# Kernel tuning notes

Measured on AMD Instinct MI355X. Metric: run time of the kernel, lower is better.

## Reference

```python
import jax, jax.numpy as jnp
import numpy as np

# dims (match init_kwargs)
B, S, HID = 2, 2048, 2048
NH = 16
DN = 128   # qk_nope_head_dim
DR = 64    # qk_rope_head_dim
DV = 128   # v_head_dim
QLR = 1536 # q_lora_rank
KVLR = 512 # kv_lora_rank
QHD = DN + DR  # 192
ROPE_BASE = 10000.0
EPS = 1e-6


def rms_norm(x, w):
    # ZeroCenteredRMSNorm: weight is zero-centered, scale = (1 + w)
    var = jnp.mean(x * x, axis=-1, keepdims=True)
    return x * jax.lax.rsqrt(var + EPS) * (1.0 + w)


def rotate_half(x):
    d = x.shape[-1] // 2
    return jnp.concatenate([-x[..., d:], x[..., :d]], axis=-1)


def deinterleave(x):
    # rearrange '(d_pairs two) -> (two d_pairs)'
    return jnp.concatenate([x[..., 0::2], x[..., 1::2]], axis=-1)


def setup_inputs() -> dict:
    key = jax.random.key(0)
    ks = jax.random.split(key, 8)
    s = 0.02
    return {
        "hidden_states": jax.random.normal(ks[0], (B, S, HID), jnp.float32),
        "position_ids": jnp.arange(S, dtype=jnp.int32),
        "Wq_down": jax.random.normal(ks[1], (HID, QLR), jnp.float32) * s,
        "q_norm_w": jnp.zeros((QLR,), jnp.float32),
        "Wq_up": jax.random.normal(ks[2], (QLR, NH * QHD), jnp.float32) * s,
        "Wkv_down": jax.random.normal(ks[3], (HID, KVLR + DR), jnp.float32) * s,
        "kv_norm_w": jnp.zeros((KVLR,), jnp.float32),
        "Wkv_up": jax.random.normal(ks[4], (KVLR, NH * (DN + DV)), jnp.float32) * s,
        "W_gate": jax.random.normal(ks[5], (HID, NH * DV), jnp.float32) * s,
        "W_out": jax.random.normal(ks[6], (NH * DV, HID), jnp.float32) * s,
    }


def reference(hidden_states, position_ids, Wq_down, q_norm_w, Wq_up,
              Wkv_down, kv_norm_w, Wkv_up, W_gate, W_out):
    bsz, q_len, _ = hidden_states.shape
    pos = jnp.broadcast_to(position_ids[None, :], (bsz, q_len))  # [b,s]

    # Q path: down-proj -> RMSNorm -> up-proj -> [b,h,s,QHD]
    q = rms_norm(hidden_states @ Wq_down, q_norm_w) @ Wq_up
    q = q.reshape(bsz, q_len, NH, QHD).transpose(0, 2, 1, 3)
    q_nope, q_rope = q[..., :DN], q[..., DN:]

    # KV path: joint down-proj -> split latent / rope key
    ckv = hidden_states @ Wkv_down                     # [b,s,KVLR+DR]
    c_kv, k_rope = ckv[..., :KVLR], ckv[..., KVLR:]
    k_rope = k_rope[:, None, :, :]                     # [b,1,s,DR]
    kv = rms_norm(c_kv, kv_norm_w) @ Wkv_up            # [b,s,NH*(DN+DV)]
    kv = kv.reshape(bsz, q_len, NH, DN + DV).transpose(0, 2, 1, 3)
    k_nope, v = kv[..., :DN], kv[..., DN:]

    # partial RoPE on rope dims (with the '(pairs two)->(two pairs)' permute)
    inv_freq = 1.0 / (ROPE_BASE ** (jnp.arange(0, DR, 2, dtype=jnp.float32) / DR))
    freqs = pos[..., None].astype(jnp.float32) * inv_freq  # [b,s,DR/2]
    emb = jnp.concatenate([freqs, freqs], axis=-1)          # [b,s,DR]
    cos = jnp.cos(emb)[:, None, :, :]                       # [b,1,s,DR]
    sin = jnp.sin(emb)[:, None, :, :]
    q_r = deinterleave(q_rope)
    k_r = deinterleave(k_rope)
    q_r = q_r * cos + rotate_half(q_r) * sin
    k_r = k_r * cos + rotate_half(k_r) * sin

    query = jnp.concatenate([q_nope, q_r], axis=-1)                       # [b,h,s,QHD]
    key = jnp.concatenate([k_nope, jnp.broadcast_to(k_r, k_nope.shape[:-1] + (DR,))], axis=-1)

    scores = jnp.einsum('bhqd,bhkd->bhqk', query, key) / np.sqrt(QHD)
    attn = jax.nn.softmax(scores, axis=-1)
    out = jnp.einsum('bhqk,bhkd->bhqd', attn, v)                          # [b,h,s,DV]
    out = out.transpose(0, 2, 1, 3)                                       # [b,s,h,DV]

    gate = jax.nn.sigmoid(hidden_states @ W_gate).reshape(bsz, q_len, NH, DV)
    out = (out * gate).reshape(bsz, q_len, NH * DV)
    return out @ W_out
```

## Files before the change

kernel.cpp:

```cpp
#include <hip/hip_runtime.h>
#include <math.h>

#define BT 2
#define SL 2048
#define HIDN 2048
#define NHEADS 16
#define DNOPE 128
#define DROPE 64
#define DVAL 128
#define QHEAD 192
#define QLRANK 1536
#define KVLRANK 512
#define TTOK (BT * SL)
#define FN 4224
#define FC_CKV 1536
#define FC_ROPE 2048
#define FC_GATE 2176

typedef unsigned short u16;
typedef u16 u16x4 __attribute__((ext_vector_type(4)));
typedef u16 u16x8 __attribute__((ext_vector_type(8)));
typedef short bf16x8 __attribute__((ext_vector_type(8)));
typedef float f32x4 __attribute__((ext_vector_type(4)));

__device__ __forceinline__ u16 f2b(float f) {
    union { float f; unsigned u; } v; v.f = f;
    unsigned r = v.u + 0x7FFFu + ((v.u >> 16) & 1u);
    return (u16)(r >> 16);
}
__device__ __forceinline__ float b2f(u16 h) {
    union { unsigned u; float f; } v; v.u = ((unsigned)h) << 16;
    return v.f;
}

__device__ __forceinline__ void gl2lds16(const u16* g, u16* l) {
    __builtin_amdgcn_global_load_lds((const __attribute__((address_space(1))) unsigned int*)g,
                                     (__attribute__((address_space(3))) unsigned int*)l, 16, 0, 0);
}

__global__ __launch_bounds__(256) void cast_k(const float* __restrict__ in, u16* __restrict__ out,
                                              int n4) {
    int i = blockIdx.x * 256 + threadIdx.x;
    const int stride = gridDim.x * 256;
    for (; i < n4; i += stride) {
        const float4 v = ((const float4*)in)[i];
        u16x4 u;
        u.x = f2b(v.x); u.y = f2b(v.y); u.z = f2b(v.z); u.w = f2b(v.w);
        ((u16x4*)out)[i] = u;
    }
}

__device__ __forceinline__ void tcast_tile(const float* __restrict__ in, u16* __restrict__ out,
                                           int R, int C, int tx, int ty, int t) {
    __shared__ u16 tile[64][72];
    const int c0 = tx * 64, r0 = ty * 64;
    const int tr = t >> 4, tc4 = (t & 15) * 4;
#pragma unroll
    for (int i = 0; i < 4; ++i) {
        const int r = tr + i * 16;
        const float4 v = *(const float4*)&in[(size_t)(r0 + r) * C + c0 + tc4];
        u16x4 u;
        u.x = f2b(v.x); u.y = f2b(v.y); u.z = f2b(v.z); u.w = f2b(v.w);
        *(u16x4*)&tile[r][tc4] = u;
    }
    __syncthreads();
#pragma unroll
    for (int i = 0; i < 4; ++i) {
        const int rr = tr + i * 16;
        u16x4 u;
        u.x = tile[tc4 + 0][rr];
        u.y = tile[tc4 + 1][rr];
        u.z = tile[tc4 + 2][rr];
        u.w = tile[tc4 + 3][rr];
        *(u16x4*)&out[(size_t)(c0 + rr) * R + r0 + tc4] = u;
    }
}

__global__ __launch_bounds__(256) void tcast_all_k(
    const float* __restrict__ Wq_down, const float* __restrict__ Wq_up,
    const float* __restrict__ Wkv_down, const float* __restrict__ Wkv_up,
    const float* __restrict__ W_gate, const float* __restrict__ W_out, u16* __restrict__ wqd_t,
    u16* __restrict__ wqu_t, u16* __restrict__ wkvd_t, u16* __restrict__ wkvu_t,
    u16* __restrict__ wg_t, u16* __restrict__ wo_t) {
    const int tid = blockIdx.x;
    const int t = threadIdx.x;
    if (tid < 768) {
        tcast_tile(Wq_down, wqd_t, 2048, 1536, tid % 24, tid / 24, t);
    } else if (tid < 1920) {
        const int i = tid - 768;
        tcast_tile(Wq_up, wqu_t, 1536, 3072, i % 48, i / 48, t);
    } else if (tid < 2208) {
        const int i = tid - 1920;
        tcast_tile(Wkv_down, wkvd_t, 2048, 576, i % 9, i / 9, t);
    } else if (tid < 2720) {
        const int i = tid - 2208;
        tcast_tile(Wkv_up, wkvu_t, 512, 4096, i % 64, i / 64, t);
    } else if (tid < 3744) {
        const int i = tid - 2720;
        tcast_tile(W_gate, wg_t, 2048, 2048, i % 32, i / 32, t);
    } else {
        const int i = tid - 3744;
        tcast_tile(W_out, wo_t, 2048, 2048, i % 32, i / 32, t);
    }
}

__global__ __launch_bounds__(256) void vtrans_k(const u16* __restrict__ kvbuf,
                                                u16* __restrict__ vT) {
    __shared__ u16 tile[64][72];
    const int bh = blockIdx.z;
    const int b = bh >> 4, h = bh & 15;
    const int s0 = blockIdx.x * 64, d0 = blockIdx.y * 64;
    const int t = threadIdx.x;
    const int tr = t >> 4, tc4 = (t & 15) * 4;
#pragma unroll
    for (int i = 0; i < 4; ++i) {
        const int s = tr + i * 16;
        *(u16x4*)&tile[s][tc4] =
            *(const u16x4*)&kvbuf[(size_t)(b * SL + s0 + s) * 4096 + h * 256 + 128 + d0 + tc4];
    }
    __syncthreads();
#pragma unroll
    for (int i = 0; i < 4; ++i) {
        const int dd = tr + i * 16;
        u16x4 u;
        u.x = tile[tc4 + 0][dd];
        u.y = tile[tc4 + 1][dd];
        u.z = tile[tc4 + 2][dd];
        u.w = tile[tc4 + 3][dd];
        *(u16x4*)&vT[(size_t)(bh * 128 + d0 + dd) * SL + s0 + tc4] = u;
    }
}

template <int EPI, int OUTF>
__global__ __launch_bounds__(256) void gemm_bf16_k(const u16* __restrict__ A,
                                                   const u16* __restrict__ Bt,
                                                   void* __restrict__ Cv, int M, int N, int K) {
    __shared__ u16 As[128 * 64];
    __shared__ u16 Bs[128 * 64];
    const int t = threadIdx.x;
    const int nx = gridDim.x;
    const int bid = blockIdx.x + nx * blockIdx.y;
    const int cpx = (nx * gridDim.y) >> 3;
    const int swz = (bid & 7) * cpx + (bid >> 3);
    const int bn = (swz % nx) * 128, bm = (swz / nx) * 128;
    const int w = t >> 6, lane = t & 63;
    const int wr = (w >> 1) * 64, wc = (w & 1) * 64;
    const int lr = lane & 15, lg = lane >> 4;

    const int srow = w * 32 + (lane >> 3);
    const int scol = ((lane & 7) ^ ((lane >> 3) & 7)) * 8;
    const u16* Ag = A + (size_t)(bm + srow) * K + scol;
    const u16* Bg = Bt + (size_t)(bn + srow) * K + scol;
    u16* Asl = As + w * 2048;
    u16* Bsl = Bs + w * 2048;

    f32x4 acc[4][4];
#pragma unroll
    for (int i = 0; i < 4; ++i)
#pragma unroll
        for (int j = 0; j < 4; ++j) acc[i][j] = 0.f;

    for (int k0 = 0; k0 < K; k0 += 64) {
        __syncthreads();
#pragma unroll
        for (int j = 0; j < 4; ++j) gl2lds16(Ag + (size_t)(j * 8) * K + k0, Asl + j * 512);
#pragma unroll
        for (int j = 0; j < 4; ++j) gl2lds16(Bg + (size_t)(j * 8) * K + k0, Bsl + j * 512);
        __syncthreads();
#pragma unroll
        for (int kk = 0; kk < 2; ++kk) {
            bf16x8 af[4], bfr[4];
#pragma unroll
            for (int mi = 0; mi < 4; ++mi) {
                const int row = wr + mi * 16 + lr;
                const int idx = (row * 64 + kk * 32 + lg * 8) ^ ((row & 7) << 3);
                af[mi] = *(const bf16x8*)&As[idx];
            }
#pragma unroll
            for (int ni = 0; ni < 4; ++ni) {
                const int row = wc + ni * 16 + lr;
                const int idx = (row * 64 + kk * 32 + lg * 8) ^ ((row & 7) << 3);
                bfr[ni] = *(const bf16x8*)&Bs[idx];
            }
#pragma unroll
            for (int mi = 0; mi < 4; ++mi)
#pragma unroll
                for (int ni = 0; ni < 4; ++ni)
                    acc[mi][ni] = __builtin_amdgcn_mfma_f32_16x16x32_bf16(af[mi], bfr[ni],
                                                                          acc[mi][ni], 0, 0, 0);
        }
    }
#pragma unroll
    for (int mi = 0; mi < 4; ++mi)
#pragma unroll
        for (int ni = 0; ni < 4; ++ni)
#pragma unroll
            for (int r = 0; r < 4; ++r) {
                const int row = bm + wr + mi * 16 + lg * 4 + r;
                const int col = bn + wc + ni * 16 + lr;
                float v = acc[mi][ni][r];
                if (EPI == 1) v = 1.f / (1.f + __expf(-v));
                if (EPI == 2 && col >= FC_GATE) v = 1.f / (1.f + __expf(-v));
                if (col < N) {
                    if (OUTF)
                        ((float*)Cv)[(size_t)row * N + col] = v;
                    else
                        ((u16*)Cv)[(size_t)row * N + col] = f2b(v);
                }
            }
}

__global__ __launch_bounds__(256) void rms2_k(const u16* __restrict__ fout,
                                              const float* __restrict__ qw,
                                              const float* __restrict__ kw, u16* __restrict__ qn,
                                              u16* __restrict__ kvn) {
    const int rid = blockIdx.x;
    const bool isq = rid < TTOK;
    const int row = isq ? rid : rid - TTOK;
    const int n = isq ? QLRANK : KVLRANK;
    const u16* x = fout + (size_t)row * FN + (isq ? 0 : FC_CKV);
    const float* w = isq ? qw : kw;
    u16* y = isq ? (qn + (size_t)row * QLRANK) : (kvn + (size_t)row * KVLRANK);
    const int t = threadIdx.x;
    float ss = 0.f;
    for (int d = t * 4; d < n; d += 1024) {
        const u16x4 u = *(const u16x4*)&x[d];
        const float a = b2f(u.x), b = b2f(u.y), c = b2f(u.z), e = b2f(u.w);
        ss += a * a + b * b + c * c + e * e;
    }
    ss += __shfl_down(ss, 32);
    ss += __shfl_down(ss, 16);
    ss += __shfl_down(ss, 8);
    ss += __shfl_down(ss, 4);
    ss += __shfl_down(ss, 2);
    ss += __shfl_down(ss, 1);
    __shared__ float red[5];
    if ((t & 63) == 0) red[t >> 6] = ss;
    __syncthreads();
    if (t == 0) red[4] = rsqrtf((red[0] + red[1] + red[2] + red[3]) / (float)n + 1e-6f);
    __syncthreads();
    const float sc = red[4];
    for (int d = t * 4; d < n; d += 1024) {
        const u16x4 u = *(const u16x4*)&x[d];
        const float4 wv = *(const float4*)&w[d];
        u16x4 o;
        o.x = f2b(b2f(u.x) * sc * (1.f + wv.x));
        o.y = f2b(b2f(u.y) * sc * (1.f + wv.y));
        o.z = f2b(b2f(u.z) * sc * (1.f + wv.z));
        o.w = f2b(b2f(u.w) * sc * (1.f + wv.w));
        *(u16x4*)&y[d] = o;
    }
}

__global__ __launch_bounds__(64) void rope_k(u16* __restrict__ q, const u16* __restrict__ fout,
                                             u16* __restrict__ kr, const int* __restrict__ pos_ids) {
    const int tok = blockIdx.x * 2 + (threadIdx.x >> 5);
    const int j = threadIdx.x & 31;
    const int s = tok & (SL - 1);
    const float pos = (float)pos_ids[s];
    const float inv = 1.f / powf(10000.f, (float)(2 * j) / 64.f);
    const float f = pos * inv;
    const float c = cosf(f), sn = sinf(f);
    const u16* kc = fout + (size_t)tok * FN + FC_ROPE;
    const unsigned kp = *(const unsigned*)&kc[2 * j];
    const float ke = b2f((u16)(kp & 0xffff)), ko = b2f((u16)(kp >> 16));
    kr[tok * 64 + j] = f2b(ke * c - ko * sn);
    kr[tok * 64 + 32 + j] = f2b(ko * c + ke * sn);
#pragma unroll
    for (int h = 0; h < NHEADS; ++h) {
        u16* qb = q + (size_t)tok * (NHEADS * QHEAD) + h * QHEAD + DNOPE;
        const unsigned qp = *(const unsigned*)&qb[2 * j];
        const float qe = b2f((u16)(qp & 0xffff)), qo = b2f((u16)(qp >> 16));
        qb[j] = f2b(qe * c - qo * sn);
        qb[32 + j] = f2b(qo * c + qe * sn);
    }
}

#define PSTR 76
__global__ __launch_bounds__(256, 2) void mla_attn_k(const u16* __restrict__ qbuf,
                                                     const u16* __restrict__ kvbuf,
                                                     const u16* __restrict__ kr,
                                                     const u16* __restrict__ vT,
                                                     const u16* __restrict__ gateb,
                                                     u16* __restrict__ outg) {
    __shared__ u16 Ks[64 * 200];
    __shared__ u16 Vt[128 * 72];
    __shared__ u16 Ps[4 * 32 * PSTR];
    const int bh = blockIdx.x;
    const int b = bh >> 4, h = bh & 15;
    const int q0 = blockIdx.y * 128;
    const int t = threadIdx.x, w = t >> 6, lane = t & 63;
    const int lr = lane & 15, lg = lane >> 4;
    const float scale = 0.07216878364870322f;

    int kRow[6], kC8[6];
#pragma unroll
    for (int c = 0; c < 6; ++c) {
        const int i = t + c * 256;
        kRow[c] = i / 24;
        kC8[c] = (i % 24) * 8;
    }
    int vRow[4], vC8[4];
#pragma unroll
    for (int c = 0; c < 4; ++c) {
        const int i = t + c * 256;
        vRow[c] = i >> 3;
        vC8[c] = (i & 7) * 8;
    }

    bf16x8 aq[2][6];
#pragma unroll
    for (int mi = 0; mi < 2; ++mi) {
        const int qrow = b * SL + q0 + w * 32 + mi * 16 + lr;
#pragma unroll
        for (int ks = 0; ks < 6; ++ks)
            aq[mi][ks] =
                *(const bf16x8*)&qbuf[(size_t)qrow * (NHEADS * QHEAD) + h * QHEAD + ks * 32 + lg * 8];
    }

    f32x4 O[2][8];
#pragma unroll
    for (int mi = 0; mi < 2; ++mi)
#pragma unroll
        for (int df = 0; df < 8; ++df) O[mi][df] = 0.f;
    float m[2][4], l[2][4];
#pragma unroll
    for (int mi = 0; mi < 2; ++mi)
#pragma unroll
        for (int r = 0; r < 4; ++r) {
            m[mi][r] = -INFINITY;
            l[mi][r] = 0.f;
        }

    u16x8 kreg[6], vreg[4];
#define ATTN_ISSUE_K(K0)                                                                     \
    {                                                                                        \
        _Pragma("unroll") for (int c = 0; c < 6; ++c) {                                      \
            const int tok = b * SL + (K0) + kRow[c];                                         \
            kreg[c] = (kC8[c] < 128)                                                         \
                          ? *(const u16x8*)&kvbuf[(size_t)tok * 4096 + h * 256 + kC8[c]]     \
                          : *(const u16x8*)&kr[(size_t)tok * 64 + (kC8[c] - 128)];           \
        }                                                                                    \
    }
#define ATTN_ISSUE_V(K0)                                                                     \
    {                                                                                        \
        _Pragma("unroll") for (int c = 0; c < 4; ++c)                                        \
            vreg[c] = *(const u16x8*)&vT[(size_t)(bh * 128 + vRow[c]) * SL + (K0) + vC8[c]]; \
    }

    ATTN_ISSUE_K(0);
    ATTN_ISSUE_V(0);

    for (int it = 0; it < SL / 64; ++it) {
        __syncthreads();
#pragma unroll
        for (int c = 0; c < 6; ++c) *(u16x8*)&Ks[kRow[c] * 200 + kC8[c]] = kreg[c];
#pragma unroll
        for (int c = 0; c < 4; ++c) *(u16x8*)&Vt[vRow[c] * 72 + vC8[c]] = vreg[c];
        __syncthreads();
        const bool more = (it + 1) < SL / 64;
        const int kn = (it + 1) * 64;
        if (more) ATTN_ISSUE_K(kn);

        f32x4 s[2][4];
#pragma unroll
        for (int mi = 0; mi < 2; ++mi)
#pragma unroll
            for (int nf = 0; nf < 4; ++nf) s[mi][nf] = 0.f;
#pragma unroll
        for (int ks = 0; ks < 6; ++ks) {
#pragma unroll
            for (int nf = 0; nf < 4; ++nf) {
                const bf16x8 bk = *(const bf16x8*)&Ks[(nf * 16 + lr) * 200 + ks * 32 + lg * 8];
                s[0][nf] = __builtin_amdgcn_mfma_f32_16x16x32_bf16(aq[0][ks], bk, s[0][nf], 0, 0, 0);
                s[1][nf] = __builtin_amdgcn_mfma_f32_16x16x32_bf16(aq[1][ks], bk, s[1][nf], 0, 0, 0);
            }
        }

        float lmv[2][4];
        float growth = -INFINITY;
#pragma unroll
        for (int mi = 0; mi < 2; ++mi)
#pragma unroll
            for (int r = 0; r < 4; ++r) {
                float lm = fmaxf(fmaxf(s[mi][0][r], s[mi][1][r]), fmaxf(s[mi][2][r], s[mi][3][r])) * scale;
                lm = fmaxf(lm, __shfl_xor(lm, 1));
                lm = fmaxf(lm, __shfl_xor(lm, 2));
                lm = fmaxf(lm, __shfl_xor(lm, 4));
                lm = fmaxf(lm, __shfl_xor(lm, 8));
                lmv[mi][r] = lm;
                growth = fmaxf(growth, lm - m[mi][r]);
            }
        const bool skip = __all(growth <= 8.f);

#pragma unroll
        for (int mi = 0; mi < 2; ++mi) {
            const int pb = w * 32 * PSTR + mi * 16 * PSTR;
#pragma unroll
            for (int r = 0; r < 4; ++r) {
                const float mn = skip ? m[mi][r] : fmaxf(m[mi][r], lmv[mi][r]);
                float p0 = __expf(s[mi][0][r] * scale - mn);
                float p1 = __expf(s[mi][1][r] * scale - mn);
                float p2 = __expf(s[mi][2][r] * scale - mn);
                float p3 = __expf(s[mi][3][r] * scale - mn);
                float ps = (p0 + p1) + (p2 + p3);
                ps += __shfl_xor(ps, 1);
                ps += __shfl_xor(ps, 2);
                ps += __shfl_xor(ps, 4);
                ps += __shfl_xor(ps, 8);
                if (skip) {
                    l[mi][r] += ps;
                } else {
                    const float al = __expf(m[mi][r] - mn);
                    l[mi][r] = l[mi][r] * al + ps;
                    m[mi][r] = mn;
#pragma unroll
                    for (int df = 0; df < 8; ++df) O[mi][df][r] *= al;
                }
                const int prow = pb + (lg * 4 + r) * PSTR + lr;
                Ps[prow] = f2b(p0);
                Ps[prow + 16] = f2b(p1);
                Ps[prow + 32] = f2b(p2);
                Ps[prow + 48] = f2b(p3);
            }
        }

        if (more) ATTN_ISSUE_V(kn);

        bf16x8 pa[2][2];
#pragma unroll
        for (int mi = 0; mi < 2; ++mi)
#pragma unroll
            for (int ks2 = 0; ks2 < 2; ++ks2)
                pa[mi][ks2] =
                    *(const bf16x8*)&Ps[w * 32 * PSTR + (mi * 16 + lr) * PSTR + ks2 * 32 + lg * 8];
#pragma unroll
        for (int df = 0; df < 8; ++df)
#pragma unroll
            for (int ks2 = 0; ks2 < 2; ++ks2) {
                const bf16x8 bv = *(const bf16x8*)&Vt[(df * 16 + lr) * 72 + ks2 * 32 + lg * 8];
                O[0][df] = __builtin_amdgcn_mfma_f32_16x16x32_bf16(pa[0][ks2], bv, O[0][df], 0, 0, 0);
                O[1][df] = __builtin_amdgcn_mfma_f32_16x16x32_bf16(pa[1][ks2], bv, O[1][df], 0, 0, 0);
            }
    }
#pragma unroll
    for (int mi = 0; mi < 2; ++mi) {
        float invl[4];
#pragma unroll
        for (int r = 0; r < 4; ++r) invl[r] = 1.f / l[mi][r];
#pragma unroll
        for (int df = 0; df < 8; ++df)
#pragma unroll
            for (int r = 0; r < 4; ++r) {
                const int qq = b * SL + q0 + w * 32 + mi * 16 + lg * 4 + r;
                const int col = h * DVAL + df * 16 + lr;
                const float o = O[mi][df][r] * invl[r];
                const float g = b2f(gateb[(size_t)qq * FN + col]);
                outg[(size_t)qq * (NHEADS * DVAL) + col] = f2b(o * g);
            }
    }
}

extern "C" void kernel_launch(void* const* d_in, const int* in_sizes, int n_in, void* d_out,
                              int out_size, void* d_ws, size_t ws_size, hipStream_t stream) {
    const float* hs = (const float*)d_in[0];
    const int* pos = (const int*)d_in[1];
    const float* Wq_down = (const float*)d_in[2];
    const float* q_norm_w = (const float*)d_in[3];
    const float* Wq_up = (const float*)d_in[4];
    const float* Wkv_down = (const float*)d_in[5];
    const float* kv_norm_w = (const float*)d_in[6];
    const float* Wkv_up = (const float*)d_in[7];
    const float* W_gate = (const float*)d_in[8];
    const float* W_out = (const float*)d_in[9];
    float* out = (float*)d_out;

    u16* p = (u16*)d_ws;
    u16* hs16 = p;      p += (size_t)TTOK * HIDN;
    u16* wdown_t = p;   p += (size_t)FN * HIDN;
    u16* wqd_t = wdown_t;
    u16* wkvd_t = wdown_t + (size_t)QLRANK * HIDN;
    u16* wg_t = wdown_t + (size_t)FC_GATE * HIDN;
    u16* wqu_t = p;     p += (size_t)(NHEADS * QHEAD) * QLRANK;
    u16* wkvu_t = p;    p += (size_t)(NHEADS * 256) * KVLRANK;
    u16* wo_t = p;      p += (size_t)HIDN * (NHEADS * DVAL);
    u16* fout = p;      p += (size_t)TTOK * FN;
    u16* qdownN = p;    p += (size_t)TTOK * QLRANK;
    u16* qbuf = p;      p += (size_t)TTOK * (NHEADS * QHEAD);
    u16* kvn = p;       p += (size_t)TTOK * KVLRANK;
    u16* kvbuf = p;     p += (size_t)TTOK * (NHEADS * 256);
    u16* krb = p;       p += (size_t)TTOK * DROPE;
    u16* vTg = p;       p += (size_t)32 * 128 * SL;
    u16* outg = p;      p += (size_t)TTOK * (NHEADS * DVAL);

    const dim3 blk(256);

    cast_k<<<dim3(2048), blk, 0, stream>>>(hs, hs16, TTOK * HIDN / 4);
    tcast_all_k<<<dim3(4768), blk, 0, stream>>>(Wq_down, Wq_up, Wkv_down, Wkv_up, W_gate, W_out,
                                                wqd_t, wqu_t, wkvd_t, wkvu_t, wg_t, wo_t);

    gemm_bf16_k<2, 0><<<dim3(FN / 128, TTOK / 128), blk, 0, stream>>>(hs16, wdown_t, fout, TTOK,
                                                                      FN, HIDN);
    rms2_k<<<dim3(2 * TTOK), blk, 0, stream>>>(fout, q_norm_w, kv_norm_w, qdownN, kvn);
    gemm_bf16_k<0, 0><<<dim3((NHEADS * QHEAD) / 128, TTOK / 128), blk, 0, stream>>>(
        qdownN, wqu_t, qbuf, TTOK, NHEADS * QHEAD, QLRANK);
    gemm_bf16_k<0, 0><<<dim3((NHEADS * 256) / 128, TTOK / 128), blk, 0, stream>>>(
        kvn, wkvu_t, kvbuf, TTOK, NHEADS * 256, KVLRANK);
    rope_k<<<dim3(TTOK / 2), dim3(64), 0, stream>>>(qbuf, fout, krb, pos);
    vtrans_k<<<dim3(SL / 64, 2, 32), blk, 0, stream>>>(kvbuf, vTg);

    mla_attn_k<<<dim3(32, SL / 128), blk, 0, stream>>>(qbuf, kvbuf, krb, vTg, fout + FC_GATE, outg);

    gemm_bf16_k<0, 1><<<dim3(HIDN / 128, TTOK / 128), blk, 0, stream>>>(outg, wo_t, out, TTOK, HIDN,
                                                                        NHEADS * DVAL);
}
```

Measured before the change: 482.0 us.

## Fuse V transpose into KV-up GEMM epilogue, merge casts, use exp2 softmax

The KV up-projection GEMM epilogue now writes K-nope into a compact buffer and V directly in transposed layout, which removes the separate vtrans kernel and the full kvbuf round trip. The hidden-state cast is folded into the weight precast kernel, saving one launch. The attention kernel pre-scales Q by scale*log2(e) at load time and uses raw v_exp_f32 (exp2), which drops per-element multiplies in the softmax. In exchange, Q is rounded to bf16 a second time after scaling, and the V stores from the GEMM epilogue are scattered 8-byte writes.

```diff
diff --git a/kernel.cpp b/kernel.cpp
--- a/kernel.cpp
+++ b/kernel.cpp
@@ -32,22 +32,15 @@
     union { unsigned u; float f; } v; v.u = ((unsigned)h) << 16;
     return v.f;
 }
+__device__ __forceinline__ float fexp2(float x) {
+    float r;
+    asm("v_exp_f32 %0, %1" : "=v"(r) : "v"(x));
+    return r;
+}
 
 __device__ __forceinline__ void gl2lds16(const u16* g, u16* l) {
     __builtin_amdgcn_global_load_lds((const __attribute__((address_space(1))) unsigned int*)g,
                                      (__attribute__((address_space(3))) unsigned int*)l, 16, 0, 0);
-}
-
-__global__ __launch_bounds__(256) void cast_k(const float* __restrict__ in, u16* __restrict__ out,
-                                              int n4) {
-    int i = blockIdx.x * 256 + threadIdx.x;
-    const int stride = gridDim.x * 256;
-    for (; i < n4; i += stride) {
-        const float4 v = ((const float4*)in)[i];
-        u16x4 u;
-        u.x = f2b(v.x); u.y = f2b(v.y); u.z = f2b(v.z); u.w = f2b(v.w);
-        ((u16x4*)out)[i] = u;
-    }
 }
 
 __device__ __forceinline__ void tcast_tile(const float* __restrict__ in, u16* __restrict__ out,
@@ -76,14 +69,25 @@
     }
 }
 
-__global__ __launch_bounds__(256) void tcast_all_k(
+__global__ __launch_bounds__(256) void precast_k(
     const float* __restrict__ Wq_down, const float* __restrict__ Wq_up,
     const float* __restrict__ Wkv_down, const float* __restrict__ Wkv_up,
-    const float* __restrict__ W_gate, const float* __restrict__ W_out, u16* __restrict__ wqd_t,
-    u16* __restrict__ wqu_t, u16* __restrict__ wkvd_t, u16* __restrict__ wkvu_t,
-    u16* __restrict__ wg_t, u16* __restrict__ wo_t) {
+    const float* __restrict__ W_gate, const float* __restrict__ W_out,
+    const float* __restrict__ hs, u16* __restrict__ wqd_t, u16* __restrict__ wqu_t,
+    u16* __restrict__ wkvd_t, u16* __restrict__ wkvu_t, u16* __restrict__ wg_t,
+    u16* __restrict__ wo_t, u16* __restrict__ hs16) {
     const int tid = blockIdx.x;
     const int t = threadIdx.x;
+    if (tid >= 4768) {
+        int i = (tid - 4768) * 256 + t;
+        for (; i < TTOK * HIDN / 4; i += 2048 * 256) {
+            const float4 v = ((const float4*)hs)[i];
+            u16x4 u;
+            u.x = f2b(v.x); u.y = f2b(v.y); u.z = f2b(v.z); u.w = f2b(v.w);
+            ((u16x4*)hs16)[i] = u;
+        }
+        return;
+    }
     if (tid < 768) {
         tcast_tile(Wq_down, wqd_t, 2048, 1536, tid % 24, tid / 24, t);
     } else if (tid < 1920) {
@@ -104,37 +108,11 @@
     }
 }
 
-__global__ __launch_bounds__(256) void vtrans_k(const u16* __restrict__ kvbuf,
-                                                u16* __restrict__ vT) {
-    __shared__ u16 tile[64][72];
-    const int bh = blockIdx.z;
-    const int b = bh >> 4, h = bh & 15;
-    const int s0 = blockIdx.x * 64, d0 = blockIdx.y * 64;
-    const int t = threadIdx.x;
-    const int tr = t >> 4, tc4 = (t & 15) * 4;
-#pragma unroll
-    for (int i = 0; i < 4; ++i) {
-        const int s = tr + i * 16;
-        *(u16x4*)&tile[s][tc4] =
-            *(const u16x4*)&kvbuf[(size_t)(b * SL + s0 + s) * 4096 + h * 256 + 128 + d0 + tc4];
-    }
-    __syncthreads();
-#pragma unroll
-    for (int i = 0; i < 4; ++i) {
-        const int dd = tr + i * 16;
-        u16x4 u;
-        u.x = tile[tc4 + 0][dd];
-        u.y = tile[tc4 + 1][dd];
-        u.z = tile[tc4 + 2][dd];
-        u.w = tile[tc4 + 3][dd];
-        *(u16x4*)&vT[(size_t)(bh * 128 + d0 + dd) * SL + s0 + tc4] = u;
-    }
-}
-
-template <int EPI, int OUTF>
+template <int MODE>
 __global__ __launch_bounds__(256) void gemm_bf16_k(const u16* __restrict__ A,
                                                    const u16* __restrict__ Bt,
-                                                   void* __restrict__ Cv, int M, int N, int K) {
+                                                   void* __restrict__ Cv, u16* __restrict__ C2,
+                                                   int M, int N, int K) {
     __shared__ u16 As[128 * 64];
     __shared__ u16 Bs[128 * 64];
     const int t = threadIdx.x;
@@ -193,21 +171,38 @@
 #pragma unroll
     for (int mi = 0; mi < 4; ++mi)
 #pragma unroll
-        for (int ni = 0; ni < 4; ++ni)
-#pragma unroll
-            for (int r = 0; r < 4; ++r) {
-                const int row = bm + wr + mi * 16 + lg * 4 + r;
-                const int col = bn + wc + ni * 16 + lr;
-                float v = acc[mi][ni][r];
-                if (EPI == 1) v = 1.f / (1.f + __expf(-v));
-                if (EPI == 2 && col >= FC_GATE) v = 1.f / (1.f + __expf(-v));
-                if (col < N) {
-                    if (OUTF)
-                        ((float*)Cv)[(size_t)row * N + col] = v;
+        for (int ni = 0; ni < 4; ++ni) {
+            const int row0 = bm + wr + mi * 16 + lg * 4;
+            const int col = bn + wc + ni * 16 + lr;
+            if (MODE == 3) {
+                const int h = col >> 8, cd = col & 255;
+                if (cd < 128) {
+#pragma unroll
+                    for (int r = 0; r < 4; ++r)
+                        ((u16*)Cv)[(size_t)(row0 + r) * 2048 + h * 128 + cd] =
+                            f2b(acc[mi][ni][r]);
+                } else {
+                    u16x4 pk;
+                    pk.x = f2b(acc[mi][ni][0]);
+                    pk.y = f2b(acc[mi][ni][1]);
+                    pk.z = f2b(acc[mi][ni][2]);
+                    pk.w = f2b(acc[mi][ni][3]);
+                    const int bb = row0 >> 11;
+                    *(u16x4*)&C2[((size_t)((bb * 16 + h) * 128 + (cd - 128))) * SL +
+                                 (row0 & (SL - 1))] = pk;
+                }
+            } else {
+#pragma unroll
+                for (int r = 0; r < 4; ++r) {
+                    float v = acc[mi][ni][r];
+                    if (MODE == 2 && col >= FC_GATE) v = 1.f / (1.f + __expf(-v));
+                    if (MODE == 1)
+                        ((float*)Cv)[(size_t)(row0 + r) * N + col] = v;
                     else
-                        ((u16*)Cv)[(size_t)row * N + col] = f2b(v);
+                        ((u16*)Cv)[(size_t)(row0 + r) * N + col] = f2b(v);
                 }
             }
+        }
 }
 
 __global__ __launch_bounds__(256) void rms2_k(const u16* __restrict__ fout,
@@ -278,7 +273,7 @@
 
 #define PSTR 76
 __global__ __launch_bounds__(256, 2) void mla_attn_k(const u16* __restrict__ qbuf,
-                                                     const u16* __restrict__ kvbuf,
+                                                     const u16* __restrict__ knope,
                                                      const u16* __restrict__ kr,
                                                      const u16* __restrict__ vT,
                                                      const u16* __restrict__ gateb,
@@ -291,7 +286,8 @@
     const int q0 = blockIdx.y * 128;
     const int t = threadIdx.x, w = t >> 6, lane = t & 63;
     const int lr = lane & 15, lg = lane >> 4;
-    const float scale = 0.07216878364870322f;
+    const float qs = 0.07216878364870322f * 1.4426950408889634f;
+    const float THR = 8.f * 1.4426950408889634f;
 
     int kRow[6], kC8[6];
 #pragma unroll
@@ -313,9 +309,14 @@
     for (int mi = 0; mi < 2; ++mi) {
         const int qrow = b * SL + q0 + w * 32 + mi * 16 + lr;
 #pragma unroll
-        for (int ks = 0; ks < 6; ++ks)
-            aq[mi][ks] =
-                *(const bf16x8*)&qbuf[(size_t)qrow * (NHEADS * QHEAD) + h * QHEAD + ks * 32 + lg * 8];
+        for (int ks = 0; ks < 6; ++ks) {
+            const u16x8 raw = *(const u16x8*)&qbuf[(size_t)qrow * (NHEADS * QHEAD) + h * QHEAD +
+                                                   ks * 32 + lg * 8];
+            bf16x8 o;
+#pragma unroll
+            for (int j = 0; j < 8; ++j) o[j] = (short)f2b(b2f(raw[j]) * qs);
+            aq[mi][ks] = o;
+        }
     }
 
     f32x4 O[2][8];
@@ -338,7 +339,7 @@
         _Pragma("unroll") for (int c = 0; c < 6; ++c) {                                      \
             const int tok = b * SL + (K0) + kRow[c];                                         \
             kreg[c] = (kC8[c] < 128)                                                         \
-                          ? *(const u16x8*)&kvbuf[(size_t)tok * 4096 + h * 256 + kC8[c]]     \
+                          ? *(const u16x8*)&knope[(size_t)tok * 2048 + h * 128 + kC8[c]]     \
                           : *(const u16x8*)&kr[(size_t)tok * 64 + (kC8[c] - 128)];           \
         }                                                                                    \
     }
@@ -383,7 +384,7 @@
         for (int mi = 0; mi < 2; ++mi)
 #pragma unroll
             for (int r = 0; r < 4; ++r) {
-                float lm = fmaxf(fmaxf(s[mi][0][r], s[mi][1][r]), fmaxf(s[mi][2][r], s[mi][3][r])) * scale;
+                float lm = fmaxf(fmaxf(s[mi][0][r], s[mi][1][r]), fmaxf(s[mi][2][r], s[mi][3][r]));
                 lm = fmaxf(lm, __shfl_xor(lm, 1));
                 lm = fmaxf(lm, __shfl_xor(lm, 2));
                 lm = fmaxf(lm, __shfl_xor(lm, 4));
@@ -391,7 +392,7 @@
                 lmv[mi][r] = lm;
                 growth = fmaxf(growth, lm - m[mi][r]);
             }
-        const bool skip = __all(growth <= 8.f);
+        const bool skip = __all(growth <= THR);
 
 #pragma unroll
         for (int mi = 0; mi < 2; ++mi) {
@@ -399,10 +400,10 @@
 #pragma unroll
             for (int r = 0; r < 4; ++r) {
                 const float mn = skip ? m[mi][r] : fmaxf(m[mi][r], lmv[mi][r]);
-                float p0 = __expf(s[mi][0][r] * scale - mn);
-                float p1 = __expf(s[mi][1][r] * scale - mn);
-                float p2 = __expf(s[mi][2][r] * scale - mn);
-                float p3 = __expf(s[mi][3][r] * scale - mn);
+                float p0 = fexp2(s[mi][0][r] - mn);
+                float p1 = fexp2(s[mi][1][r] - mn);
+                float p2 = fexp2(s[mi][2][r] - mn);
+                float p3 = fexp2(s[mi][3][r] - mn);
                 float ps = (p0 + p1) + (p2 + p3);
                 ps += __shfl_xor(ps, 1);
                 ps += __shfl_xor(ps, 2);
@@ -411,7 +412,7 @@
                 if (skip) {
                     l[mi][r] += ps;
                 } else {
-                    const float al = __expf(m[mi][r] - mn);
+                    const float al = fexp2(m[mi][r] - mn);
                     l[mi][r] = l[mi][r] * al + ps;
                     m[mi][r] = mn;
 #pragma unroll
@@ -488,29 +489,27 @@
     u16* qdownN = p;    p += (size_t)TTOK * QLRANK;
     u16* qbuf = p;      p += (size_t)TTOK * (NHEADS * QHEAD);
     u16* kvn = p;       p += (size_t)TTOK * KVLRANK;
-    u16* kvbuf = p;     p += (size_t)TTOK * (NHEADS * 256);
+    u16* knope = p;     p += (size_t)TTOK * (NHEADS * DNOPE);
     u16* krb = p;       p += (size_t)TTOK * DROPE;
     u16* vTg = p;       p += (size_t)32 * 128 * SL;
     u16* outg = p;      p += (size_t)TTOK * (NHEADS * DVAL);
 
     const dim3 blk(256);
 
-    cast_k<<<dim3(2048), blk, 0, stream>>>(hs, hs16, TTOK * HIDN / 4);
-    tcast_all_k<<<dim3(4768), blk, 0, stream>>>(Wq_down, Wq_up, Wkv_down, Wkv_up, W_gate, W_out,
-                                                wqd_t, wqu_t, wkvd_t, wkvu_t, wg_t, wo_t);
-
-    gemm_bf16_k<2, 0><<<dim3(FN / 128, TTOK / 128), blk, 0, stream>>>(hs16, wdown_t, fout, TTOK,
-                                                                      FN, HIDN);
+    precast_k<<<dim3(6816), blk, 0, stream>>>(Wq_down, Wq_up, Wkv_down, Wkv_up, W_gate, W_out, hs,
+                                              wqd_t, wqu_t, wkvd_t, wkvu_t, wg_t, wo_t, hs16);
+
+    gemm_bf16_k<2><<<dim3(FN / 128, TTOK / 128), blk, 0, stream>>>(hs16, wdown_t, fout, nullptr,
+                                                                   TTOK, FN, HIDN);
     rms2_k<<<dim3(2 * TTOK), blk, 0, stream>>>(fout, q_norm_w, kv_norm_w, qdownN, kvn);
-    gemm_bf16_k<0, 0><<<dim3((NHEADS * QHEAD) / 128, TTOK / 128), blk, 0, stream>>>(
-        qdownN, wqu_t, qbuf, TTOK, NHEADS * QHEAD, QLRANK);
-    gemm_bf16_k<0, 0><<<dim3((NHEADS * 256) / 128, TTOK / 128), blk, 0, stream>>>(
-        kvn, wkvu_t, kvbuf, TTOK, NHEADS * 256, KVLRANK);
+    gemm_bf16_k<0><<<dim3((NHEADS * QHEAD) / 128, TTOK / 128), blk, 0, stream>>>(
+        qdownN, wqu_t, qbuf, nullptr, TTOK, NHEADS * QHEAD, QLRANK);
+    gemm_bf16_k<3><<<dim3((NHEADS * 256) / 128, TTOK / 128), blk, 0, stream>>>(
+        kvn, wkvu_t, knope, vTg, TTOK, NHEADS * 256, KVLRANK);
     rope_k<<<dim3(TTOK / 2), dim3(64), 0, stream>>>(qbuf, fout, krb, pos);
-    vtrans_k<<<dim3(SL / 64, 2, 32), blk, 0, stream>>>(kvbuf, vTg);
-
-    mla_attn_k<<<dim3(32, SL / 128), blk, 0, stream>>>(qbuf, kvbuf, krb, vTg, fout + FC_GATE, outg);
-
-    gemm_bf16_k<0, 1><<<dim3(HIDN / 128, TTOK / 128), blk, 0, stream>>>(outg, wo_t, out, TTOK, HIDN,
-                                                                        NHEADS * DVAL);
-}
+
+    mla_attn_k<<<dim3(32, SL / 128), blk, 0, stream>>>(qbuf, knope, krb, vTg, fout + FC_GATE, outg);
+
+    gemm_bf16_k<1><<<dim3(HIDN / 128, TTOK / 128), blk, 0, stream>>>(outg, wo_t, out, nullptr, TTOK,
+                                                                     HIDN, NHEADS * DVAL);
+}
```

Result: faster. 466.0 us, median of 2 (-3.3%).
